# Optimization experiments

Hardware: AMD Instinct MI355X
Metric: run time of the kernel (lower is better)

Reference implementation:

```python
import jax, jax.numpy as jnp
import numpy as np

N_NODES = 100000
N_EDGES = 1600000
D = 64
N_RELS = 200
LEAKY_SLOPE = 0.01


def setup_inputs() -> dict:
    key = jax.random.key(0)
    ks = jax.random.split(key, 12)
    def xavier(k, shape):
        gain = float(np.sqrt(2.0))  # calculate_gain('relu')
        bound = gain * float(np.sqrt(6.0 / (shape[0] + shape[1])))
        return jax.random.uniform(k, shape, jnp.float32, -bound, bound)
    return {
        "h": jax.random.normal(ks[0], (N_NODES, D), jnp.float32),
        "rel_emb": jax.random.normal(ks[1], (N_RELS, D), jnp.float32),
        "weight_neighbor": xavier(ks[2], (2 * D, D)),
        "attn_w": (xavier(ks[3], (3 * D, 1))).reshape(3 * D),
        "delta": jnp.ones((1,), jnp.float32),
        "loop_weight": xavier(ks[4], (D, D)),
        "evolve_loop_weight": xavier(ks[5], (D, D)),
        "etime": jax.random.uniform(ks[6], (N_EDGES,), jnp.float32),
        "src": jax.random.randint(ks[7], (N_EDGES,), 0, N_NODES),
        "dst": jax.random.randint(ks[8], (N_EDGES,), 0, N_NODES),
        "etype": jax.random.randint(ks[9], (N_EDGES,), 0, N_RELS),
    }


def reference(h, rel_emb, weight_neighbor, attn_w, delta, loop_weight,
              evolve_loop_weight, etime, src, dst, etype):
    N, d = h.shape
    # cat(src_h, rel) @ W  ==  src_h @ W[:d] + rel @ W[d:]  (precompute per node / per relation)
    hW = h @ weight_neighbor[:d]                 # [N, d]
    relW = rel_emb @ weight_neighbor[d:]         # [R, d]
    # attn_fc(cat(src_h, dst_h, rel)) == per-node/per-rel scalar contributions
    a1, a2, a3 = attn_w[:d], attn_w[d:2 * d], attn_w[2 * d:]
    s_src = h @ a1                               # [N]
    s_dst = h @ a2                               # [N]
    s_rel = rel_emb @ a3                         # [R]
    e = jax.nn.leaky_relu(s_src[src] + s_dst[dst] + s_rel[etype], LEAKY_SLOPE)  # [E]
    k = -etime * delta[0]                        # [E]
    scores = k * e                               # [E]
    # segment softmax over in-edges of each destination node
    m = jax.ops.segment_max(scores, dst, num_segments=N)          # [N]
    ex = jnp.exp(scores - m[dst])                                  # [E]
    den = jax.ops.segment_sum(ex, dst, num_segments=N)             # [N]
    w = ex / den[dst]                                              # [E]
    msg = hW[src] + relW[etype]                                    # [E, d]
    agg = jax.ops.segment_sum(w[:, None] * msg, dst, num_segments=N)  # [N, d]
    # nodes with no in-edges keep original h (DGL update_all semantics)
    deg = jax.ops.segment_sum(jnp.ones_like(scores), dst, num_segments=N)
    has_in = (deg > 0)[:, None]
    loop = jnp.where(has_in, h @ loop_weight, h @ evolve_loop_weight)
    node_repr = jnp.where(has_in, agg, h) + loop
    return node_repr
```

## Files before the change

kernel.cpp:

```cpp
#include <hip/hip_runtime.h>
#include <hip/hip_bf16.h>

#define N_NODES 100000
#define N_EDGES 1600000
#define D       64
#define N_RELS  200
#define LEAKY   0.01f
#define NBUCK      782
#define BUCK_SHIFT 7
#define BUCK_MASK  127
#define NPB        128
#define CAP        3072
#define BIN_CHUNK  2048
#define NBIN       ((N_EDGES + BIN_CHUNK - 1) / BIN_CHUNK)

typedef __hip_bfloat16 bf16;

__device__ __forceinline__ float b2f(bf16 x) { return __bfloat162float(x); }
__device__ __forceinline__ bf16  f2b(float x) { return __float2bfloat16(x); }

__device__ __forceinline__ float ldf(const void* p, long i, int bf) {
    return bf ? __bfloat162float(((const bf16*)p)[i]) : ((const float*)p)[i];
}
__device__ __forceinline__ int probe_bf(const void* delta) {
    return ((const unsigned short*)delta)[0] == 0x3F80 ? 1 : 0;
}

__device__ __forceinline__ int rl_i(int v, int l) {
    return __builtin_amdgcn_readlane(v, l);
}
__device__ __forceinline__ float rl_f(float v, int l) {
    return __int_as_float(__builtin_amdgcn_readlane(__float_as_int(v), l));
}

__global__ __launch_bounds__(512, 4) void k_fused_proj(const void* __restrict__ h,
                                                       const void* __restrict__ wn,
                                                       const void* __restrict__ attn,
                                                       const void* __restrict__ delta,
                                                       const void* __restrict__ rel_emb,
                                                       const int* __restrict__ dst,
                                                       bf16* __restrict__ hWb,
                                                       float* __restrict__ s_src,
                                                       float* __restrict__ s_dst,
                                                       float* __restrict__ relW,
                                                       float* __restrict__ s_rel,
                                                       int* __restrict__ bcnt) {
    __shared__ int bh[NBUCK];
    const int bf = probe_bf(delta);
    const int wave = threadIdx.x >> 6;
    const int lane = threadIdx.x & 63;
    const int gw = blockIdx.x * 8 + wave;
    const int nwaves = gridDim.x * 8;
    float wreg[D];
    #pragma unroll
    for (int k = 0; k < D; k++) wreg[k] = ldf(wn, (long)k * D + lane, bf);
    const float a1 = ldf(attn, lane, bf);
    const float a2 = ldf(attn, D + lane, bf);
    for (int base = gw * 8; base < N_NODES; base += nwaves * 8) {
        float hv[8], acc[8];
        #pragma unroll
        for (int j = 0; j < 8; j++) {
            hv[j] = ldf(h, (long)(base + j) * D + lane, bf);
            acc[j] = 0.f;
        }
        #pragma unroll
        for (int j = 0; j < 8; j++) {
            float p1 = hv[j] * a1, p2 = hv[j] * a2;
            #pragma unroll
            for (int off = 32; off; off >>= 1) { p1 += __shfl_xor(p1, off); p2 += __shfl_xor(p2, off); }
            if (lane == 0) { s_src[base + j] = p1; s_dst[base + j] = p2; }
        }
        #pragma unroll
        for (int k = 0; k < D; k++) {
            float w = wreg[k];
            #pragma unroll
            for (int j = 0; j < 8; j++) acc[j] += rl_f(hv[j], k) * w;
        }
        #pragma unroll
        for (int j = 0; j < 8; j++) hWb[(long)(base + j) * D + lane] = f2b(acc[j]);
    }
    const float a3 = ldf(attn, 2 * D + lane, bf);
    for (int r = gw; r < N_RELS; r += nwaves) {
        float rv = ldf(rel_emb, (long)r * D + lane, bf);
        float p3 = rv * a3;
        #pragma unroll
        for (int off = 32; off; off >>= 1) p3 += __shfl_xor(p3, off);
        if (lane == 0) s_rel[r] = p3;
        float acc = 0.f;
        #pragma unroll
        for (int k = 0; k < D; k++) {
            acc += rl_f(rv, k) * ldf(wn, (long)(D + k) * D + lane, bf);
        }
        relW[r * D + lane] = acc;
    }
    for (int t = threadIdx.x; t < NBUCK; t += 512) bh[t] = 0;
    __syncthreads();
    for (int t = blockIdx.x * 512 + threadIdx.x; t < N_EDGES; t += gridDim.x * 512)
        atomicAdd(&bh[dst[t] >> BUCK_SHIFT], 1);
    __syncthreads();
    for (int t = threadIdx.x; t < NBUCK; t += 512) {
        int v = bh[t];
        if (v) atomicAdd(&bcnt[t], v);
    }
}

__global__ __launch_bounds__(1024) void k_bscan(const int* __restrict__ bcnt,
                                                int* __restrict__ bbase,
                                                int* __restrict__ bcursor) {
    __shared__ int s[1024];
    const int tid = threadIdx.x;
    int v = (tid < NBUCK) ? bcnt[tid] : 0;
    s[tid] = v;
    __syncthreads();
    for (int off = 1; off < 1024; off <<= 1) {
        int t = (tid >= off) ? s[tid - off] : 0;
        __syncthreads();
        s[tid] += t;
        __syncthreads();
    }
    if (tid < NBUCK) {
        int e = s[tid] - v;
        bbase[tid] = e;
        bcursor[tid] = e;
    }
    if (tid == 1023) bbase[NBUCK] = s[1023];
}

__global__ __launch_bounds__(512, 6) void k_bin(const float* __restrict__ s_src,
                                                const float* __restrict__ s_dst,
                                                const float* __restrict__ s_rel,
                                                const void* __restrict__ etime,
                                                const void* __restrict__ delta,
                                                const int* __restrict__ src,
                                                const int* __restrict__ dst,
                                                const int* __restrict__ etype,
                                                int* __restrict__ bcursor,
                                                int2* __restrict__ payl) {
    __shared__ int lh[NBUCK];
    __shared__ int gbase[NBUCK];
    const int bf = probe_bf(delta);
    const float df = ldf(delta, 0, bf);
    const int tid = threadIdx.x;
    const int base = blockIdx.x * BIN_CHUNK;
    for (int t = tid; t < NBUCK; t += 512) lh[t] = 0;
    __syncthreads();
    int2 rc[4];
    int rk[4], bk[4];
    #pragma unroll
    for (int j = 0; j < 4; j++) {
        int e = base + j * 512 + tid;
        bk[j] = -1;
        if (e < N_EDGES) {
            int s = src[e], d = dst[e], r = etype[e];
            float scv = s_src[s] + s_dst[d] + s_rel[r];
            float lre = scv > 0.f ? scv : LEAKY * scv;
            float score = (-ldf(etime, e, bf) * df) * lre;
            rc[j].x = __float_as_int(__expf(score));
            rc[j].y = s | (r << 17) | ((d & BUCK_MASK) << 25);
            int b = d >> BUCK_SHIFT;
            bk[j] = b;
            rk[j] = atomicAdd(&lh[b], 1);
        }
    }
    __syncthreads();
    for (int t = tid; t < NBUCK; t += 512) {
        int v = lh[t];
        if (v) gbase[t] = atomicAdd(&bcursor[t], v);
    }
    __syncthreads();
    #pragma unroll
    for (int j = 0; j < 4; j++) {
        if (bk[j] >= 0) payl[gbase[bk[j]] + rk[j]] = rc[j];
    }
}

__global__ __launch_bounds__(512, 4) void k_loop(const void* __restrict__ h,
                                                 const void* __restrict__ loopW,
                                                 const void* __restrict__ delta,
                                                 float* __restrict__ L) {
    const int bf = probe_bf(delta);
    const int wave = threadIdx.x >> 6;
    const int lane = threadIdx.x & 63;
    const int gw = blockIdx.x * 8 + wave;
    const int nwaves = gridDim.x * 8;
    float wreg[D];
    #pragma unroll
    for (int k = 0; k < D; k++) wreg[k] = ldf(loopW, (long)k * D + lane, bf);
    for (int base = gw * 8; base < N_NODES; base += nwaves * 8) {
        float hv[8], acc[8];
        #pragma unroll
        for (int j = 0; j < 8; j++) {
            hv[j] = ldf(h, (long)(base + j) * D + lane, bf);
            acc[j] = 0.f;
        }
        #pragma unroll
        for (int k = 0; k < D; k++) {
            float w = wreg[k];
            #pragma unroll
            for (int j = 0; j < 8; j++) acc[j] += rl_f(hv[j], k) * w;
        }
        #pragma unroll
        for (int j = 0; j < 8; j++) L[(long)(base + j) * D + lane] = acc[j];
    }
}

__global__ __launch_bounds__(512, 6) void k_bagg(const int2* __restrict__ payl,
                                                 const int* __restrict__ bbase,
                                                 const bf16* __restrict__ hWb,
                                                 const float* __restrict__ relW,
                                                 const void* __restrict__ h,
                                                 const void* __restrict__ evolveW,
                                                 const float* __restrict__ L,
                                                 const void* __restrict__ delta,
                                                 float* __restrict__ out) {
    __shared__ int2 recs[CAP];
    __shared__ int cnt[NPB], off[NPB], fc[NPB];
    const int bf = probe_bf(delta);
    const int tid = threadIdx.x;
    const int b = blockIdx.x;
    const int n0 = b << BUCK_SHIFT;
    const int s0 = bbase[b], s1 = bbase[b + 1];
    const int run = s1 - s0;
    if (tid < NPB) { cnt[tid] = 0; fc[tid] = 0; }
    __syncthreads();
    for (int i = tid; i < run; i += 512)
        atomicAdd(&cnt[((unsigned)payl[s0 + i].y) >> 25], 1);
    __syncthreads();
    if (tid < NPB) off[tid] = cnt[tid];
    __syncthreads();
    for (int o = 1; o < NPB; o <<= 1) {
        int t = 0;
        if (tid < NPB && tid >= o) t = off[tid - o];
        __syncthreads();
        if (tid < NPB) off[tid] += t;
        __syncthreads();
    }
    if (tid < NPB) off[tid] -= cnt[tid];
    __syncthreads();
    for (int i = tid; i < run; i += 512) {
        int2 r = payl[s0 + i];
        int z = ((unsigned)r.y) >> 25;
        int pos = off[z] + atomicAdd(&fc[z], 1);
        if (pos < CAP) recs[pos] = r;
    }
    __syncthreads();
    const int wave = tid >> 6, lane = tid & 63;
    const int grp = lane >> 4, sub = lane & 15;
    const unsigned sub8 = (unsigned)sub << 3;
    const unsigned sub16 = (unsigned)sub << 4;
    for (int t = 0; t < 16; ++t) {
        const int z = wave * 16 + t;
        const int i = n0 + z;
        if (i >= N_NODES) break;
        const int d = cnt[z], o = off[z];
        if (d > 0) {
            float ax = 0.f, ay = 0.f, az = 0.f, aw = 0.f, ws = 0.f;
            if (o + d <= CAP) {
                #pragma unroll 2
                for (int j = 0; j < d; j += 4) {
                    int jj = j + grp;
                    int2 rr = (jj < d) ? recs[o + jj] : make_int2(0, 0);
                    float w = __int_as_float(rr.x);
                    int p = rr.y;
                    unsigned hoff = ((unsigned)(p & 0x1FFFF) << 7) + sub8;
                    unsigned roff = ((((unsigned)p >> 17) & 0xFFu) << 8) + sub16;
                    uint2  hw = *(const uint2*) ((const char*)hWb  + hoff);
                    float4 rw = *(const float4*)((const char*)relW + roff);
                    float f0 = __uint_as_float(hw.x << 16);
                    float f1 = __uint_as_float(hw.x & 0xFFFF0000u);
                    float f2 = __uint_as_float(hw.y << 16);
                    float f3 = __uint_as_float(hw.y & 0xFFFF0000u);
                    ax += w * (f0 + rw.x);
                    ay += w * (f1 + rw.y);
                    az += w * (f2 + rw.z);
                    aw += w * (f3 + rw.w);
                    ws += w;
                }
            } else {
                for (int j = 0; j < run; j += 4) {
                    int jj = j + grp;
                    if (jj < run) {
                        int2 rr = payl[s0 + jj];
                        if ((int)(((unsigned)rr.y) >> 25) == z) {
                            float w = __int_as_float(rr.x);
                            int p = rr.y;
                            unsigned hoff = ((unsigned)(p & 0x1FFFF) << 7) + sub8;
                            unsigned roff = ((((unsigned)p >> 17) & 0xFFu) << 8) + sub16;
                            uint2  hw = *(const uint2*) ((const char*)hWb  + hoff);
                            float4 rw = *(const float4*)((const char*)relW + roff);
                            ax += w * (__uint_as_float(hw.x << 16) + rw.x);
                            ay += w * (__uint_as_float(hw.x & 0xFFFF0000u) + rw.y);
                            az += w * (__uint_as_float(hw.y << 16) + rw.z);
                            aw += w * (__uint_as_float(hw.y & 0xFFFF0000u) + rw.w);
                            ws += w;
                        }
                    }
                }
            }
            ax += __shfl_xor(ax, 16); ax += __shfl_xor(ax, 32);
            ay += __shfl_xor(ay, 16); ay += __shfl_xor(ay, 32);
            az += __shfl_xor(az, 16); az += __shfl_xor(az, 32);
            aw += __shfl_xor(aw, 16); aw += __shfl_xor(aw, 32);
            ws += __shfl_xor(ws, 16); ws += __shfl_xor(ws, 32);
            if (grp == 0) {
                const float inv = 1.f / ws;
                const float4 l4 = *(const float4*)(L + (long)i * D + sub * 4);
                float4 r;
                r.x = ax * inv + l4.x;
                r.y = ay * inv + l4.y;
                r.z = az * inv + l4.z;
                r.w = aw * inv + l4.w;
                *(float4*)(out + (long)i * D + sub * 4) = r;
            }
        } else {
            float hv = ldf(h, (long)i * D + lane, bf);
            float acc = hv;
            for (int k = 0; k < D; k++)
                acc += rl_f(hv, k) * ldf(evolveW, (long)k * D + lane, bf);
            out[(long)i * D + lane] = acc;
        }
    }
}

__global__ __launch_bounds__(256) void k_fallback(float* __restrict__ out) {
    int t = blockIdx.x * blockDim.x + threadIdx.x;
    if (t < N_NODES * D) out[t] = 0.f;
}

extern "C" void kernel_launch(void* const* d_in, const int* in_sizes, int n_in,
                              void* d_out, int out_size, void* d_ws, size_t ws_size,
                              hipStream_t stream) {
    const void* h       = d_in[0];
    const void* rel_emb = d_in[1];
    const void* wn      = d_in[2];
    const void* attn    = d_in[3];
    const void* delta   = d_in[4];
    const void* loopW   = d_in[5];
    const void* evolveW = d_in[6];
    const void* etime   = d_in[7];
    const int*  src     = (const int*)d_in[8];
    const int*  dst     = (const int*)d_in[9];
    const int*  etype   = (const int*)d_in[10];
    float* out = (float*)d_out;

    char* ws = (char*)d_ws;
    size_t off = 0;
    auto alloc = [&](size_t bytes) -> void* {
        off = (off + 255) & ~(size_t)255;
        void* p = ws + off;
        off += bytes;
        return p;
    };
    int2*  payl    = (int2*) alloc((size_t)N_EDGES * 8);
    float* L       = (float*)alloc((size_t)N_NODES * D * 4);
    bf16*  hWb     = (bf16*) alloc((size_t)N_NODES * D * 2);
    float* relW    = (float*)alloc((size_t)N_RELS * D * 4);
    float* s_src   = (float*)alloc((size_t)N_NODES * 4);
    float* s_dst   = (float*)alloc((size_t)N_NODES * 4);
    float* s_rel   = (float*)alloc((size_t)N_RELS * 4);
    int*   bcnt    = (int*)  alloc((size_t)NBUCK * 4);
    int*   bbase   = (int*)  alloc((size_t)(NBUCK + 1) * 4);
    int*   bcursor = (int*)  alloc((size_t)NBUCK * 4);

    if (ws_size < off) {
        k_fallback<<<(N_NODES * D + 255) / 256, 256, 0, stream>>>(out);
        return;
    }

    hipMemsetAsync(bcnt, 0, (size_t)NBUCK * 4, stream);
    k_fused_proj<<<782, 512, 0, stream>>>(h, wn, attn, delta, rel_emb, dst,
                                          hWb, s_src, s_dst, relW, s_rel, bcnt);
    k_bscan<<<1, 1024, 0, stream>>>(bcnt, bbase, bcursor);
    k_bin<<<NBIN, 512, 0, stream>>>(s_src, s_dst, s_rel, etime, delta,
                                    src, dst, etype, bcursor, payl);
    k_loop<<<782, 512, 0, stream>>>(h, loopW, delta, L);
    k_bagg<<<NBUCK, 512, 0, stream>>>(payl, bbase, hWb, relW, h, evolveW, L, delta, out);
}
```

Baseline: 289.7 us.

## Compute node projection and loop GEMMs with bf16 MFMA using hi/lo split

```diff
diff --git a/kernel.cpp b/kernel.cpp
--- a/kernel.cpp
+++ b/kernel.cpp
@@ -15,9 +15,20 @@
 #define NBIN       ((N_EDGES + BIN_CHUNK - 1) / BIN_CHUNK)
 
 typedef __hip_bfloat16 bf16;
+typedef __attribute__((ext_vector_type(8))) short bf16x8;
+typedef __attribute__((ext_vector_type(4))) float f32x4;
 
 __device__ __forceinline__ float b2f(bf16 x) { return __bfloat162float(x); }
 __device__ __forceinline__ bf16  f2b(float x) { return __float2bfloat16(x); }
+
+__device__ __forceinline__ unsigned short f2bs(float x) {
+    unsigned u = __float_as_uint(x);
+    unsigned r = (u + 0x7FFFu + ((u >> 16) & 1u)) >> 16;
+    return (unsigned short)r;
+}
+__device__ __forceinline__ float bs2f(unsigned short s) {
+    return __uint_as_float(((unsigned)s) << 16);
+}
 
 __device__ __forceinline__ float ldf(const void* p, long i, int bf) {
     return bf ? __bfloat162float(((const bf16*)p)[i]) : ((const float*)p)[i];
@@ -51,33 +62,52 @@
     const int lane = threadIdx.x & 63;
     const int gw = blockIdx.x * 8 + wave;
     const int nwaves = gridDim.x * 8;
-    float wreg[D];
-    #pragma unroll
-    for (int k = 0; k < D; k++) wreg[k] = ldf(wn, (long)k * D + lane, bf);
-    const float a1 = ldf(attn, lane, bf);
-    const float a2 = ldf(attn, D + lane, bf);
-    for (int base = gw * 8; base < N_NODES; base += nwaves * 8) {
-        float hv[8], acc[8];
-        #pragma unroll
-        for (int j = 0; j < 8; j++) {
-            hv[j] = ldf(h, (long)(base + j) * D + lane, bf);
-            acc[j] = 0.f;
-        }
-        #pragma unroll
-        for (int j = 0; j < 8; j++) {
-            float p1 = hv[j] * a1, p2 = hv[j] * a2;
-            #pragma unroll
-            for (int off = 32; off; off >>= 1) { p1 += __shfl_xor(p1, off); p2 += __shfl_xor(p2, off); }
-            if (lane == 0) { s_src[base + j] = p1; s_dst[base + j] = p2; }
-        }
-        #pragma unroll
-        for (int k = 0; k < D; k++) {
-            float w = wreg[k];
-            #pragma unroll
-            for (int j = 0; j < 8; j++) acc[j] += rl_f(hv[j], k) * w;
-        }
-        #pragma unroll
-        for (int j = 0; j < 8; j++) hWb[(long)(base + j) * D + lane] = f2b(acc[j]);
+    const int rc16 = lane & 15;
+    const int kg   = lane >> 4;
+    {
+        const int base = gw * 16;
+        if (base < N_NODES) {
+            bf16x8 Bf[4][2];
+            #pragma unroll
+            for (int c = 0; c < 4; c++)
+                #pragma unroll
+                for (int t = 0; t < 2; t++)
+                    #pragma unroll
+                    for (int j = 0; j < 8; j++)
+                        Bf[c][t][j] = (short)f2bs(ldf(wn, (long)(t * 32 + kg * 8 + j) * D + c * 16 + rc16, bf));
+            bf16x8 Ahi[2], Alo[2];
+            float p1 = 0.f, p2 = 0.f;
+            #pragma unroll
+            for (int t = 0; t < 2; t++) {
+                #pragma unroll
+                for (int j = 0; j < 8; j++) {
+                    float hv = ldf(h, (long)(base + rc16) * D + t * 32 + kg * 8 + j, bf);
+                    p1 += hv * ldf(attn, t * 32 + kg * 8 + j, bf);
+                    p2 += hv * ldf(attn, D + t * 32 + kg * 8 + j, bf);
+                    unsigned short hi = f2bs(hv);
+                    Ahi[t][j] = (short)hi;
+                    Alo[t][j] = (short)f2bs(hv - bs2f(hi));
+                }
+            }
+            p1 += __shfl_xor(p1, 16); p1 += __shfl_xor(p1, 32);
+            p2 += __shfl_xor(p2, 16); p2 += __shfl_xor(p2, 32);
+            if (lane < 16) { s_src[base + rc16] = p1; s_dst[base + rc16] = p2; }
+            f32x4 acc[4];
+            #pragma unroll
+            for (int c = 0; c < 4; c++) acc[c] = (f32x4){0.f, 0.f, 0.f, 0.f};
+            #pragma unroll
+            for (int t = 0; t < 2; t++)
+                #pragma unroll
+                for (int c = 0; c < 4; c++) {
+                    acc[c] = __builtin_amdgcn_mfma_f32_16x16x32_bf16(Ahi[t], Bf[c][t], acc[c], 0, 0, 0);
+                    acc[c] = __builtin_amdgcn_mfma_f32_16x16x32_bf16(Alo[t], Bf[c][t], acc[c], 0, 0, 0);
+                }
+            #pragma unroll
+            for (int c = 0; c < 4; c++)
+                #pragma unroll
+                for (int r = 0; r < 4; r++)
+                    hWb[(long)(base + kg * 4 + r) * D + c * 16 + rc16] = f2b(acc[c][r]);
+        }
     }
     const float a3 = ldf(attn, 2 * D + lane, bf);
     for (int r = gw; r < N_RELS; r += nwaves) {
@@ -182,26 +212,43 @@
     const int wave = threadIdx.x >> 6;
     const int lane = threadIdx.x & 63;
     const int gw = blockIdx.x * 8 + wave;
-    const int nwaves = gridDim.x * 8;
-    float wreg[D];
-    #pragma unroll
-    for (int k = 0; k < D; k++) wreg[k] = ldf(loopW, (long)k * D + lane, bf);
-    for (int base = gw * 8; base < N_NODES; base += nwaves * 8) {
-        float hv[8], acc[8];
+    const int rc16 = lane & 15;
+    const int kg   = lane >> 4;
+    const int base = gw * 16;
+    if (base >= N_NODES) return;
+    bf16x8 Bf[4][2];
+    #pragma unroll
+    for (int c = 0; c < 4; c++)
+        #pragma unroll
+        for (int t = 0; t < 2; t++)
+            #pragma unroll
+            for (int j = 0; j < 8; j++)
+                Bf[c][t][j] = (short)f2bs(ldf(loopW, (long)(t * 32 + kg * 8 + j) * D + c * 16 + rc16, bf));
+    bf16x8 Ahi[2], Alo[2];
+    #pragma unroll
+    for (int t = 0; t < 2; t++)
         #pragma unroll
         for (int j = 0; j < 8; j++) {
-            hv[j] = ldf(h, (long)(base + j) * D + lane, bf);
-            acc[j] = 0.f;
-        }
-        #pragma unroll
-        for (int k = 0; k < D; k++) {
-            float w = wreg[k];
-            #pragma unroll
-            for (int j = 0; j < 8; j++) acc[j] += rl_f(hv[j], k) * w;
-        }
-        #pragma unroll
-        for (int j = 0; j < 8; j++) L[(long)(base + j) * D + lane] = acc[j];
-    }
+            float hv = ldf(h, (long)(base + rc16) * D + t * 32 + kg * 8 + j, bf);
+            unsigned short hi = f2bs(hv);
+            Ahi[t][j] = (short)hi;
+            Alo[t][j] = (short)f2bs(hv - bs2f(hi));
+        }
+    f32x4 acc[4];
+    #pragma unroll
+    for (int c = 0; c < 4; c++) acc[c] = (f32x4){0.f, 0.f, 0.f, 0.f};
+    #pragma unroll
+    for (int t = 0; t < 2; t++)
+        #pragma unroll
+        for (int c = 0; c < 4; c++) {
+            acc[c] = __builtin_amdgcn_mfma_f32_16x16x32_bf16(Ahi[t], Bf[c][t], acc[c], 0, 0, 0);
+            acc[c] = __builtin_amdgcn_mfma_f32_16x16x32_bf16(Alo[t], Bf[c][t], acc[c], 0, 0, 0);
+        }
+    #pragma unroll
+    for (int c = 0; c < 4; c++)
+        #pragma unroll
+        for (int r = 0; r < 4; r++)
+            L[(long)(base + kg * 4 + r) * D + c * 16 + rc16] = acc[c][r];
 }
 
 __global__ __launch_bounds__(512, 6) void k_bagg(const int2* __restrict__ payl,
```

Result: faster. 273.4 us (median of 2 runs) (-5.6%).
